# Kernel tuning notes

Hardware: AMD Instinct MI355X
Metric: run time of the kernel (lower is better)

The kernel has to match this reference:

```python
import jax, jax.numpy as jnp
from jax import lax
import numpy as np

STRIDES = (2, 2)
PADDING = 'SAME'
EPS = 1e-05


def setup_inputs() -> dict:
    key = jax.random.key(0)
    k1, k2, k3 = jax.random.split(key, 3)
    x = jax.random.normal(k1, (16, 64, 64, 256), dtype=jnp.float32)
    # flax default conv kernel init ~ lecun_normal; plain normal scaled is fine for a math reference
    kernel = jax.random.normal(k2, (4, 4, 256, 128), dtype=jnp.float32) * 0.05
    bias = jax.random.normal(k3, (128,), dtype=jnp.float32) * 0.01
    alpha = jnp.ones((1,), dtype=jnp.float32)
    return {'x': x, 'kernel': kernel, 'bias': bias, 'alpha': alpha}


def reference(x, kernel, bias, alpha):
    # x: [B, H, W, Cin] NHWC; kernel: [kh, kw, Cin, Cout]
    out_features = kernel.shape[-1]

    # main transposed conv: dot-product map  [B, H*2, W*2, Cout]
    dot = lax.conv_transpose(x, kernel, STRIDES, PADDING, transpose_kernel=False)

    # patch squared-sum map: conv_transpose of x**2 with an all-ones kernel
    # of shape kernel_size + (Cin, 1); broadcast over Cout (same math as jnp.repeat)
    ones_k = jnp.ones(kernel.shape[:-1] + (1,), dtype=kernel.dtype)
    patch_sq = lax.conv_transpose(x * x, ones_k, STRIDES, PADDING, transpose_kernel=False)  # [B, H', W', 1]

    # per-filter kernel squared norm, reduced over (kh, kw, Cin) -> [Cout]
    k_sq = jnp.sum(kernel * kernel, axis=(0, 1, 2))

    # ||x_patch - W||^2 = sum(x^2) + sum(W^2) - 2 * <x, W>
    dist_sq = patch_sq + k_sq - 2.0 * dot

    y = (dot * dot) / (dist_sq + EPS)
    y = y + bias  # broadcast over [B, H', W', Cout]

    nf = jnp.float32(out_features)
    scale = (jnp.sqrt(nf) / jnp.log1p(nf)) ** alpha  # alpha shape (1,) broadcasts
    return y * scale
```

## Files before the change

kernel.cpp:

```cpp
#include <hip/hip_runtime.h>
#include <cstdint>
#include <cstddef>

#define CIN   256
#define COUT  128

typedef float  f32x4  __attribute__((ext_vector_type(4)));
typedef __bf16 bf16x8 __attribute__((ext_vector_type(8)));

#define XPAD_BYTES (16ull*66*66*256*2)
#define WF_OFF     XPAD_BYTES
#define WF_BYTES   (16ull*8*4*128*8*2)
#define SPAD_OFF   (WF_OFF + WF_BYTES)
#define SPAD_BYTES (16ull*66*66*4)
#define KSQ_OFF    (SPAD_OFF + SPAD_BYTES)
#define WS_NEEDED  (KSQ_OFF + 512)

__device__ __forceinline__ unsigned short f2bf(float f) {
  unsigned int u = __float_as_uint(f);
  u += 0x7fffu + ((u >> 16) & 1u);
  return (unsigned short)(u >> 16);
}

__device__ __forceinline__ void async16(const void* lds, const void* g) {
  __builtin_amdgcn_global_load_lds(
      (const __attribute__((address_space(1))) unsigned int*)g,
      (__attribute__((address_space(3))) unsigned int*)lds, 16, 0, 0);
}

__global__ __launch_bounds__(256) void prep_x(
    const float* __restrict__ x, unsigned short* __restrict__ xpad,
    float* __restrict__ spad)
{
  int wave = threadIdx.x >> 6, lane = threadIdx.x & 63;
  int p = blockIdx.x * 4 + wave;
  int b = p / 4356;
  int rem = p - b * 4356;
  int iyp = rem / 66, ixp = rem - iyp * 66;
  bool interior = (iyp >= 1 && iyp <= 64 && ixp >= 1 && ixp <= 64);
  f32x4 v = {0.f, 0.f, 0.f, 0.f};
  if (interior) {
    const float* src = x + (((size_t)b*64 + (iyp-1))*64 + (ixp-1))*CIN + lane*4;
    v = *(const f32x4*)src;
  }
  ushort4 h;
  h.x = f2bf(v.x); h.y = f2bf(v.y); h.z = f2bf(v.z); h.w = f2bf(v.w);
  *(ushort4*)(xpad + (size_t)p*CIN + lane*4) = h;
  float s = v.x*v.x + v.y*v.y + v.z*v.z + v.w*v.w;
  #pragma unroll
  for (int off = 32; off > 0; off >>= 1) s += __shfl_down(s, off);
  if (lane == 0) spad[p] = s;
}

__global__ __launch_bounds__(256) void prep_w2(
    const float* __restrict__ w, unsigned short* __restrict__ wf,
    float* __restrict__ ksq)
{
  int blk = blockIdx.x;
  int tap = blk >> 3, c8 = blk & 7;
  int t = threadIdx.x;
  #pragma unroll
  for (int rr = 0; rr < 2; ++rr) {
    int row = rr*256 + t;
    int q = row >> 7, co = row & 127;
    float s = 0.f;
    union { unsigned short u[8]; uint4 v; } hh;
    #pragma unroll
    for (int e = 0; e < 8; ++e) {
      int ci = c8*32 + q*8 + e;
      float v = w[((size_t)tap*256 + ci)*COUT + co];
      s += v*v;
      hh.u[e] = f2bf(v);
    }
    *(uint4*)(wf + ((size_t)blk*4 + q)*128*8 + (size_t)co*8) = hh.v;
    atomicAdd(ksq + co, s);
  }
}

__global__ __launch_bounds__(256, 2) void yat_main(
    const unsigned short* __restrict__ xpad,
    const unsigned short* __restrict__ wf,
    const float* __restrict__ spad,
    const float* __restrict__ ksq,
    const float* __restrict__ bias,
    const float* __restrict__ alpha,
    float* __restrict__ out)
{
  __shared__ __align__(16) unsigned short xs[2][4224];
  __shared__ float srow[132];

  int orig = blockIdx.x;
  int bid = (orig & 7) * 256 + (orig >> 3);
  int py = bid & 1, u = (bid >> 1) & 63, b = bid >> 7;
  int t = threadIdx.x, wave = t >> 6, lane = t & 63;
  int px = wave >> 1, coh = wave & 1;
  int l15 = lane & 15, l4 = lane >> 4;

  if (t < 132) {
    int r = t / 66, c = t - r*66;
    srow[t] = spad[((size_t)b*66 + (u + py) + r)*66 + c];
  }

  const size_t xrow = ((size_t)b*66 + (u + py)) * 66 * CIN;

  size_t soff0, soff1, tailoff = 0;
  {
    int s = t;
    int a = s / 264; int r2 = s - a*264;
    int q = r2 / 66; int c = r2 - q*66;
    soff0 = xrow + (size_t)(a*66 + c)*CIN + q*8;
    s = 256 + t;
    a = s / 264; r2 = s - a*264;
    q = r2 / 66; c = r2 - q*66;
    soff1 = xrow + (size_t)(a*66 + c)*CIN + q*8;
  }
  if (t < 16) {
    int s2 = 248 + t;
    int q = s2 / 66, c = s2 - q*66;
    tailoff = xrow + (size_t)(66 + c)*CIN + q*8;
  }

  const unsigned short* abase = &xs[0][((size_t)l4*66 + l15 + px)*8];
  const unsigned short* wb =
      wf + ((size_t)l4*128 + coh*64 + l15)*8 + (size_t)(py*4 + px)*32768;

  f32x4 acc[4][4];
  #pragma unroll
  for (int i = 0; i < 4; ++i)
    #pragma unroll
    for (int j = 0; j < 4; ++j)
      acc[i][j] = (f32x4){0.f, 0.f, 0.f, 0.f};

  bf16x8 B0[2][4], B1[2][4];

#define LOAD_B(BANK, AA, C8)                                               \
  {                                                                        \
    _Pragma("unroll")                                                      \
    for (int bb = 0; bb < 2; ++bb)                                         \
      _Pragma("unroll")                                                    \
      for (int nt = 0; nt < 4; ++nt)                                       \
        BANK[bb][nt] = *(const bf16x8*)(                                   \
            wb + (size_t)(AA)*262144 + (size_t)bb*65536 +                  \
                 (size_t)(C8)*4096 + nt*128);                              \
  }

#define STAGE_DMA(NB, CI0)                                                 \
  {                                                                        \
    async16(&xs[NB][(size_t)(0*256 + wave*64)*8], xpad + soff0 + (CI0));   \
    async16(&xs[NB][(size_t)(1*256 + wave*64)*8], xpad + soff1 + (CI0));   \
  }

#define COMPUTE_HALF(BUF, AA, BANK)                                        \
  {                                                                        \
    bf16x8 Af[2][4];                                                       \
    _Pragma("unroll")                                                      \
    for (int bb = 0; bb < 2; ++bb)                                         \
      _Pragma("unroll")                                                    \
      for (int mt = 0; mt < 4; ++mt)                                       \
        Af[bb][mt] = *(const bf16x8*)(abase + (size_t)(BUF)*4224 +         \
            (size_t)((AA)*264 + mt*16 + bb)*8);                            \
    __builtin_amdgcn_s_setprio(1);                                         \
    _Pragma("unroll")                                                      \
    for (int bb = 0; bb < 2; ++bb)                                         \
      _Pragma("unroll")                                                    \
      for (int mt = 0; mt < 4; ++mt)                                       \
        _Pragma("unroll")                                                  \
        for (int nt = 0; nt < 4; ++nt)                                     \
          acc[mt][nt] = __builtin_amdgcn_mfma_f32_16x16x32_bf16(           \
              Af[bb][mt], BANK[bb][nt], acc[mt][nt], 0, 0, 0);             \
    __builtin_amdgcn_s_setprio(0);                                         \
  }

  STAGE_DMA(0, 0);
  uint4 tv;
  if (t < 16) tv = *(const uint4*)(xpad + tailoff);
  LOAD_B(B0, 0, 0);
  if (t < 16) *(uint4*)&xs[0][(size_t)(512 + t)*8] = tv;
  asm volatile("s_waitcnt vmcnt(8) lgkmcnt(0)" ::: "memory");
  __builtin_amdgcn_s_barrier();

  #pragma unroll
  for (int c8 = 0; c8 < 8; ++c8) {
    const int buf = c8 & 1;
    LOAD_B(B1, 1, c8);
    if (c8 < 7) {
      STAGE_DMA(buf ^ 1, (c8 + 1) * 32);
      if (t < 16) tv = *(const uint4*)(xpad + tailoff + (c8 + 1) * 32);
    }
    __builtin_amdgcn_sched_barrier(0);
    COMPUTE_HALF(buf, 0, B0);
    if (c8 < 7) LOAD_B(B0, 0, c8 + 1);
    __builtin_amdgcn_sched_barrier(0);
    COMPUTE_HALF(buf, 1, B1);
    if (c8 < 7) {
      if (t < 16) *(uint4*)&xs[buf ^ 1][(size_t)(512 + t)*8] = tv;
      asm volatile("s_waitcnt vmcnt(8) lgkmcnt(0)" ::: "memory");
      __builtin_amdgcn_s_barrier();
    }
  }

#undef LOAD_B
#undef STAGE_DMA
#undef COMPUTE_HALF

  float scale = powf(sqrtf(128.f) / log1pf(128.f), alpha[0]);
  int oy = 2*u + py;
  float kq[4], bi[4];
  #pragma unroll
  for (int nt = 0; nt < 4; ++nt) {
    int n = coh*64 + nt*16 + l15;
    kq[nt] = ksq[n]; bi[nt] = bias[n];
  }
  size_t orow = ((size_t)b*128 + oy) * 128 * COUT;
  #pragma unroll
  for (int mt = 0; mt < 4; ++mt) {
    #pragma unroll
    for (int r = 0; r < 4; ++r) {
      int v = mt*16 + l4*4 + r;
      float ps = srow[v+px] + srow[v+px+1] + srow[66 + v+px] + srow[66 + v+px+1];
      #pragma unroll
      for (int nt = 0; nt < 4; ++nt) {
        float dot = acc[mt][nt][r];
        float dist = ps + kq[nt] - 2.f*dot + 1e-5f;
        float y = (dot*dot/dist + bi[nt]) * scale;
        int n = coh*64 + nt*16 + l15;
        out[orow + (size_t)(2*v + px)*COUT + n] = y;
      }
    }
  }
}

__global__ __launch_bounds__(256) void fb_ksq(const float* __restrict__ w,
                                              float* __restrict__ ksq) {
  __shared__ float red[256];
  int co = blockIdx.x, t = threadIdx.x;
  float s = 0.f;
  for (int j = t; j < 4096; j += 256) { float v = w[(size_t)j*COUT + co]; s += v*v; }
  red[t] = s; __syncthreads();
  for (int off = 128; off > 0; off >>= 1) {
    if (t < off) red[t] += red[t + off];
    __syncthreads();
  }
  if (t == 0) ksq[co] = red[0];
}

__global__ __launch_bounds__(256) void fb_main(
    const float* __restrict__ x, const float* __restrict__ w,
    const float* __restrict__ bias, const float* __restrict__ alpha,
    const float* __restrict__ ksq, float* __restrict__ out)
{
  size_t idx = (size_t)blockIdx.x * 256 + threadIdx.x;
  int co = (int)(idx & 127);
  int ox = (int)((idx >> 7) & 127);
  int oy = (int)((idx >> 14) & 127);
  int b  = (int)(idx >> 21);
  int py = oy & 1, px = ox & 1, u = oy >> 1, v = ox >> 1;
  float dot = 0.f, ps = 0.f;
  for (int a = 0; a < 2; ++a) {
    int iy = u + py + a - 1;
    if (iy < 0 || iy > 63) continue;
    for (int b2 = 0; b2 < 2; ++b2) {
      int ix = v + px + b2 - 1;
      if (ix < 0 || ix > 63) continue;
      const float* xp = x + (((size_t)b*64 + iy)*64 + ix)*CIN;
      const float* wp = w + ((size_t)((py + 2*a)*4 + (px + 2*b2))*CIN)*COUT + co;
      for (int ci = 0; ci < CIN; ++ci) {
        float xv = xp[ci];
        dot += xv * wp[(size_t)ci*COUT];
        ps  += xv * xv;
      }
    }
  }
  float dist = ps + ksq[co] - 2.f*dot + 1e-5f;
  float scale = powf(sqrtf(128.f) / log1pf(128.f), alpha[0]);
  out[idx] = (dot*dot/dist + bias[co]) * scale;
}

extern "C" void kernel_launch(void* const* d_in, const int* in_sizes, int n_in,
                              void* d_out, int out_size, void* d_ws, size_t ws_size,
                              hipStream_t stream)
{
  const float* x     = (const float*)d_in[0];
  const float* w     = (const float*)d_in[1];
  const float* bias  = (const float*)d_in[2];
  const float* alpha = (const float*)d_in[3];
  float* out = (float*)d_out;

  if (ws_size < WS_NEEDED) {
    float* ksq = (float*)d_ws;
    fb_ksq<<<128, 256, 0, stream>>>(w, ksq);
    fb_main<<<131072, 256, 0, stream>>>(x, w, bias, alpha, ksq, out);
    return;
  }

  unsigned short* xpad = (unsigned short*)d_ws;
  unsigned short* wfp  = (unsigned short*)((char*)d_ws + WF_OFF);
  float* spad = (float*)((char*)d_ws + SPAD_OFF);
  float* ksq  = (float*)((char*)d_ws + KSQ_OFF);

  hipMemsetAsync(ksq, 0, 512, stream);
  prep_x<<<17424, 256, 0, stream>>>(x, xpad, spad);
  prep_w2<<<128, 256, 0, stream>>>(w, wfp, ksq);
  yat_main<<<2048, 256, 0, stream>>>(xpad, wfp, spad, ksq, bias, alpha, out);
}
```

Before: 121.3 us.

## Pre-swizzle padded input into MFMA fragment layout and drop LDS staging

The x-preprocessing kernel now writes one padded row per block through LDS into a [b][row][ci/8][col][8] bf16 layout. The main GEMM kernel can then load A fragments directly from global memory with 16-byte vector loads, which removes the LDS double buffer, the async DMA and the per-stage barriers. Occupancy hint rises to 3 blocks per CU. In exchange, A operands are served from global memory and cache instead of shared LDS, so overlapping rows read by neighbouring blocks rely on L2 hits and latency is only hidden by occupancy.

```diff
diff --git a/kernel.cpp b/kernel.cpp
--- a/kernel.cpp
+++ b/kernel.cpp
@@ -8,8 +8,8 @@
 typedef float  f32x4  __attribute__((ext_vector_type(4)));
 typedef __bf16 bf16x8 __attribute__((ext_vector_type(8)));
 
-#define XPAD_BYTES (16ull*66*66*256*2)
-#define WF_OFF     XPAD_BYTES
+#define XF_BYTES   (16ull*66*32*66*8*2)
+#define WF_OFF     XF_BYTES
 #define WF_BYTES   (16ull*8*4*128*8*2)
 #define SPAD_OFF   (WF_OFF + WF_BYTES)
 #define SPAD_BYTES (16ull*66*66*4)
@@ -22,34 +22,50 @@
   return (unsigned short)(u >> 16);
 }
 
-__device__ __forceinline__ void async16(const void* lds, const void* g) {
-  __builtin_amdgcn_global_load_lds(
-      (const __attribute__((address_space(1))) unsigned int*)g,
-      (__attribute__((address_space(3))) unsigned int*)lds, 16, 0, 0);
-}
-
-__global__ __launch_bounds__(256) void prep_x(
-    const float* __restrict__ x, unsigned short* __restrict__ xpad,
+__global__ __launch_bounds__(256) void prep_x2(
+    const float* __restrict__ x, unsigned short* __restrict__ xf,
     float* __restrict__ spad)
 {
-  int wave = threadIdx.x >> 6, lane = threadIdx.x & 63;
-  int p = blockIdx.x * 4 + wave;
-  int b = p / 4356;
-  int rem = p - b * 4356;
-  int iyp = rem / 66, ixp = rem - iyp * 66;
-  bool interior = (iyp >= 1 && iyp <= 64 && ixp >= 1 && ixp <= 64);
-  f32x4 v = {0.f, 0.f, 0.f, 0.f};
+  __shared__ __align__(16) unsigned short lw[66*258 + 8];
+  int blk = blockIdx.x;
+  int b = blk / 66, row = blk - b*66;
+  int t = threadIdx.x, wave = t >> 6, lane = t & 63;
+  bool interior = (row >= 1 && row <= 64);
+  int iy = row - 1;
+
   if (interior) {
-    const float* src = x + (((size_t)b*64 + (iyp-1))*64 + (ixp-1))*CIN + lane*4;
-    v = *(const f32x4*)src;
-  }
-  ushort4 h;
-  h.x = f2bf(v.x); h.y = f2bf(v.y); h.z = f2bf(v.z); h.w = f2bf(v.w);
-  *(ushort4*)(xpad + (size_t)p*CIN + lane*4) = h;
-  float s = v.x*v.x + v.y*v.y + v.z*v.z + v.w*v.w;
-  #pragma unroll
-  for (int off = 32; off > 0; off >>= 1) s += __shfl_down(s, off);
-  if (lane == 0) spad[p] = s;
+    #pragma unroll
+    for (int p = 0; p < 16; ++p) {
+      int cx = 4*p + wave;
+      f32x4 v = *(const f32x4*)(x + (((size_t)b*64 + iy)*64 + cx)*CIN + lane*4);
+      ushort4 h; h.x=f2bf(v.x); h.y=f2bf(v.y); h.z=f2bf(v.z); h.w=f2bf(v.w);
+      *(ushort4*)&lw[(size_t)(cx+1)*258 + lane*4] = h;
+      float s = v.x*v.x + v.y*v.y + v.z*v.z + v.w*v.w;
+      #pragma unroll
+      for (int off = 32; off > 0; off >>= 1) s += __shfl_down(s, off);
+      if (lane == 0) spad[(size_t)blk*66 + cx + 1] = s;
+    }
+    if (t < 2) spad[(size_t)blk*66 + t*65] = 0.f;
+    if (t < 64) {
+      int col = (t & 1) * 65, q = t >> 1;
+      *(uint4*)&lw[(size_t)col*258 + q*8] = (uint4){0,0,0,0};
+    }
+  } else {
+    if (t < 66) spad[(size_t)blk*66 + t] = 0.f;
+  }
+  __syncthreads();
+
+  size_t obase = (size_t)blk * 32 * 66 * 8;
+  #pragma unroll
+  for (int k = 0; k < 9; ++k) {
+    int un = k*256 + t;
+    if (un < 2112) {
+      int q = un / 66, col = un - q*66;
+      uint4 val = interior ? *(uint4*)&lw[(size_t)col*258 + q*8]
+                           : (uint4){0u,0u,0u,0u};
+      *(uint4*)(xf + obase + (size_t)un*8) = val;
+    }
+  }
 }
 
 __global__ __launch_bounds__(256) void prep_w2(
@@ -77,8 +93,8 @@
   }
 }
 
-__global__ __launch_bounds__(256, 2) void yat_main(
-    const unsigned short* __restrict__ xpad,
+__global__ __launch_bounds__(256, 3) void yat_main(
+    const unsigned short* __restrict__ xf,
     const unsigned short* __restrict__ wf,
     const float* __restrict__ spad,
     const float* __restrict__ ksq,
@@ -86,7 +102,6 @@
     const float* __restrict__ alpha,
     float* __restrict__ out)
 {
-  __shared__ __align__(16) unsigned short xs[2][4224];
   __shared__ float srow[132];
 
   int orig = blockIdx.x;
@@ -101,26 +116,8 @@
     srow[t] = spad[((size_t)b*66 + (u + py) + r)*66 + c];
   }
 
-  const size_t xrow = ((size_t)b*66 + (u + py)) * 66 * CIN;
-
-  size_t soff0, soff1, tailoff = 0;
-  {
-    int s = t;
-    int a = s / 264; int r2 = s - a*264;
-    int q = r2 / 66; int c = r2 - q*66;
-    soff0 = xrow + (size_t)(a*66 + c)*CIN + q*8;
-    s = 256 + t;
-    a = s / 264; r2 = s - a*264;
-    q = r2 / 66; c = r2 - q*66;
-    soff1 = xrow + (size_t)(a*66 + c)*CIN + q*8;
-  }
-  if (t < 16) {
-    int s2 = 248 + t;
-    int q = s2 / 66, c = s2 - q*66;
-    tailoff = xrow + (size_t)(66 + c)*CIN + q*8;
-  }
-
-  const unsigned short* abase = &xs[0][((size_t)l4*66 + l15 + px)*8];
+  const unsigned short* ab =
+      xf + ((((size_t)b*66 + (u + py))*32 + l4)*66 + px + l15)*8;
   const unsigned short* wb =
       wf + ((size_t)l4*128 + coh*64 + l15)*8 + (size_t)(py*4 + px)*32768;
 
@@ -144,64 +141,42 @@
                  (size_t)(C8)*4096 + nt*128);                              \
   }
 
-#define STAGE_DMA(NB, CI0)                                                 \
+#define COMPUTE_HALF(AA, BANK, C8)                                         \
   {                                                                        \
-    async16(&xs[NB][(size_t)(0*256 + wave*64)*8], xpad + soff0 + (CI0));   \
-    async16(&xs[NB][(size_t)(1*256 + wave*64)*8], xpad + soff1 + (CI0));   \
-  }
-
-#define COMPUTE_HALF(BUF, AA, BANK)                                        \
-  {                                                                        \
-    bf16x8 Af[2][4];                                                       \
     _Pragma("unroll")                                                      \
-    for (int bb = 0; bb < 2; ++bb)                                         \
+    for (int bb = 0; bb < 2; ++bb) {                                       \
+      bf16x8 Af[4];                                                        \
       _Pragma("unroll")                                                    \
       for (int mt = 0; mt < 4; ++mt)                                       \
-        Af[bb][mt] = *(const bf16x8*)(abase + (size_t)(BUF)*4224 +         \
-            (size_t)((AA)*264 + mt*16 + bb)*8);                            \
-    __builtin_amdgcn_s_setprio(1);                                         \
-    _Pragma("unroll")                                                      \
-    for (int bb = 0; bb < 2; ++bb)                                         \
+        Af[mt] = *(const bf16x8*)(ab + (size_t)(AA)*16896 +                \
+            (size_t)(C8)*2112 + (mt*16 + bb)*8);                           \
+      __builtin_amdgcn_s_setprio(1);                                       \
       _Pragma("unroll")                                                    \
       for (int mt = 0; mt < 4; ++mt)                                       \
         _Pragma("unroll")                                                  \
         for (int nt = 0; nt < 4; ++nt)                                     \
           acc[mt][nt] = __builtin_amdgcn_mfma_f32_16x16x32_bf16(           \
-              Af[bb][mt], BANK[bb][nt], acc[mt][nt], 0, 0, 0);             \
-    __builtin_amdgcn_s_setprio(0);                                         \
-  }
-
-  STAGE_DMA(0, 0);
-  uint4 tv;
-  if (t < 16) tv = *(const uint4*)(xpad + tailoff);
+              Af[mt], BANK[bb][nt], acc[mt][nt], 0, 0, 0);                 \
+      __builtin_amdgcn_s_setprio(0);                                       \
+    }                                                                      \
+  }
+
   LOAD_B(B0, 0, 0);
-  if (t < 16) *(uint4*)&xs[0][(size_t)(512 + t)*8] = tv;
-  asm volatile("s_waitcnt vmcnt(8) lgkmcnt(0)" ::: "memory");
-  __builtin_amdgcn_s_barrier();
-
   #pragma unroll
   for (int c8 = 0; c8 < 8; ++c8) {
-    const int buf = c8 & 1;
     LOAD_B(B1, 1, c8);
-    if (c8 < 7) {
-      STAGE_DMA(buf ^ 1, (c8 + 1) * 32);
-      if (t < 16) tv = *(const uint4*)(xpad + tailoff + (c8 + 1) * 32);
-    }
     __builtin_amdgcn_sched_barrier(0);
-    COMPUTE_HALF(buf, 0, B0);
+    COMPUTE_HALF(0, B0, c8);
     if (c8 < 7) LOAD_B(B0, 0, c8 + 1);
     __builtin_amdgcn_sched_barrier(0);
-    COMPUTE_HALF(buf, 1, B1);
-    if (c8 < 7) {
-      if (t < 16) *(uint4*)&xs[buf ^ 1][(size_t)(512 + t)*8] = tv;
-      asm volatile("s_waitcnt vmcnt(8) lgkmcnt(0)" ::: "memory");
-      __builtin_amdgcn_s_barrier();
-    }
+    COMPUTE_HALF(1, B1, c8);
+    __builtin_amdgcn_sched_barrier(0);
   }
 
 #undef LOAD_B
-#undef STAGE_DMA
 #undef COMPUTE_HALF
+
+  __syncthreads();
 
   float scale = powf(sqrtf(128.f) / log1pf(128.f), alpha[0]);
   int oy = 2*u + py;
@@ -293,13 +268,13 @@
     return;
   }
 
-  unsigned short* xpad = (unsigned short*)d_ws;
-  unsigned short* wfp  = (unsigned short*)((char*)d_ws + WF_OFF);
+  unsigned short* xfp = (unsigned short*)d_ws;
+  unsigned short* wfp = (unsigned short*)((char*)d_ws + WF_OFF);
   float* spad = (float*)((char*)d_ws + SPAD_OFF);
   float* ksq  = (float*)((char*)d_ws + KSQ_OFF);
 
   hipMemsetAsync(ksq, 0, 512, stream);
-  prep_x<<<17424, 256, 0, stream>>>(x, xpad, spad);
+  prep_x2<<<1056, 256, 0, stream>>>(x, xfp, spad);
   prep_w2<<<128, 256, 0, stream>>>(w, wfp, ksq);
-  yat_main<<<2048, 256, 0, stream>>>(xpad, wfp, spad, ksq, bias, alpha, out);
-}
+  yat_main<<<2048, 256, 0, stream>>>(xfp, wfp, spad, ksq, bias, alpha, out);
+}
```

Result: no change. 121.5 us (+0.2%).

## Triple-buffer LDS staging with hand-scheduled inline-asm loads in GEMM main loop

Applied to the files above, without the earlier changes.

The main transposed-conv GEMM loop moves from double to triple LDS buffering. It is fully unrolled with inline-asm global_load_dwordx4 and ds_read_b128 plus explicit vmcnt and lgkmcnt waits, so x-tile DMA runs two stages ahead and the weight fragments are prefetched. The kernel-norm computation moves from atomics in prep_w2, which needed a preceding memset, to the dedicated reduction kernel. The tighter schedule is meant to hide global latency better, at the cost of more LDS per block, which could reduce occupancy, and fragile hand-counted wait values.

```diff
diff --git a/kernel.cpp b/kernel.cpp
--- a/kernel.cpp
+++ b/kernel.cpp
@@ -7,6 +7,7 @@
 
 typedef float  f32x4  __attribute__((ext_vector_type(4)));
 typedef __bf16 bf16x8 __attribute__((ext_vector_type(8)));
+typedef unsigned int u32x4 __attribute__((ext_vector_type(4)));
 
 #define XPAD_BYTES (16ull*66*66*256*2)
 #define WF_OFF     XPAD_BYTES
@@ -53,8 +54,7 @@
 }
 
 __global__ __launch_bounds__(256) void prep_w2(
-    const float* __restrict__ w, unsigned short* __restrict__ wf,
-    float* __restrict__ ksq)
+    const float* __restrict__ w, unsigned short* __restrict__ wf)
 {
   int blk = blockIdx.x;
   int tap = blk >> 3, c8 = blk & 7;
@@ -63,18 +63,28 @@
   for (int rr = 0; rr < 2; ++rr) {
     int row = rr*256 + t;
     int q = row >> 7, co = row & 127;
-    float s = 0.f;
     union { unsigned short u[8]; uint4 v; } hh;
     #pragma unroll
     for (int e = 0; e < 8; ++e) {
       int ci = c8*32 + q*8 + e;
-      float v = w[((size_t)tap*256 + ci)*COUT + co];
-      s += v*v;
-      hh.u[e] = f2bf(v);
+      hh.u[e] = f2bf(w[((size_t)tap*256 + ci)*COUT + co]);
     }
     *(uint4*)(wf + ((size_t)blk*4 + q)*128*8 + (size_t)co*8) = hh.v;
-    atomicAdd(ksq + co, s);
-  }
+  }
+}
+
+__global__ __launch_bounds__(256) void fb_ksq(const float* __restrict__ w,
+                                              float* __restrict__ ksq) {
+  __shared__ float red[256];
+  int co = blockIdx.x, t = threadIdx.x;
+  float s = 0.f;
+  for (int j = t; j < 4096; j += 256) { float v = w[(size_t)j*COUT + co]; s += v*v; }
+  red[t] = s; __syncthreads();
+  for (int off = 128; off > 0; off >>= 1) {
+    if (t < off) red[t] += red[t + off];
+    __syncthreads();
+  }
+  if (t == 0) ksq[co] = red[0];
 }
 
 __global__ __launch_bounds__(256, 2) void yat_main(
@@ -86,7 +96,7 @@
     const float* __restrict__ alpha,
     float* __restrict__ out)
 {
-  __shared__ __align__(16) unsigned short xs[2][4224];
+  __shared__ __align__(16) unsigned short xs[3][4224];
   __shared__ float srow[132];
 
   int orig = blockIdx.x;
@@ -103,7 +113,7 @@
 
   const size_t xrow = ((size_t)b*66 + (u + py)) * 66 * CIN;
 
-  size_t soff0, soff1, tailoff = 0;
+  size_t soff0, soff1, tailoff;
   {
     int s = t;
     int a = s / 264; int r2 = s - a*264;
@@ -113,14 +123,13 @@
     a = s / 264; r2 = s - a*264;
     q = r2 / 66; c = r2 - q*66;
     soff1 = xrow + (size_t)(a*66 + c)*CIN + q*8;
-  }
-  if (t < 16) {
-    int s2 = 248 + t;
-    int q = s2 / 66, c = s2 - q*66;
-    tailoff = xrow + (size_t)(66 + c)*CIN + q*8;
-  }
-
-  const unsigned short* abase = &xs[0][((size_t)l4*66 + l15 + px)*8];
+    int s2 = 248 + (t & 15);
+    int q2 = s2 / 66, c2 = s2 - q2*66;
+    tailoff = xrow + (size_t)(66 + c2)*CIN + q2*8;
+  }
+
+  unsigned ab_lds = (unsigned)(unsigned long long)(&xs[0][0])
+                    + (unsigned)((l4*66 + l15 + px) * 16);
   const unsigned short* wb =
       wf + ((size_t)l4*128 + coh*64 + l15)*8 + (size_t)(py*4 + px)*32768;
 
@@ -131,77 +140,127 @@
     for (int j = 0; j < 4; ++j)
       acc[i][j] = (f32x4){0.f, 0.f, 0.f, 0.f};
 
-  bf16x8 B0[2][4], B1[2][4];
-
-#define LOAD_B(BANK, AA, C8)                                               \
+  u32x4 B0[2][4], B1[2][4];
+  u32x4 Af[2][4];
+  u32x4 tvA, tvB;
+
+#define SB  __builtin_amdgcn_sched_barrier(0)
+#define BAR __builtin_amdgcn_s_barrier()
+#define VMW(N) do { asm volatile("s_waitcnt vmcnt(" #N ")" ::: "memory"); SB; } while (0)
+#define LGK(N) do { asm volatile("s_waitcnt lgkmcnt(" #N ")" ::: "memory"); SB; } while (0)
+
+#define GLB(dst, base, off)                                                \
+  asm volatile("global_load_dwordx4 %0, %1, off offset:%c2"                \
+               : "=v"(dst) : "v"(base), "i"(off))
+
+#define DSR(dst, off)                                                      \
+  asm volatile("ds_read_b128 %0, %1 offset:%c2"                            \
+               : "=v"(dst) : "v"(ab_lds), "i"(off))
+
+#define STAGE(BUF, K, TV)                                                  \
+  {                                                                        \
+    async16(&xs[BUF][(size_t)(0*256 + wave*64)*8], xpad + soff0 + (K)*32); \
+    async16(&xs[BUF][(size_t)(1*256 + wave*64)*8], xpad + soff1 + (K)*32); \
+    SB;                                                                    \
+    GLB(TV, (const char*)(xpad + tailoff + (K)*32), 0);                    \
+    SB;                                                                    \
+  }
+
+#define TAILW(BUF, TV)                                                     \
+  { if (t < 16) *((u32x4*)&xs[BUF][(size_t)(512 + t)*8]) = TV; }
+
+#define ISSUEB(BANK, AA, C8)                                               \
+  {                                                                        \
+    const char* pb0 = (const char*)wb + (AA)*524288 + (C8)*8192;           \
+    const char* pb1 = pb0 + 131072;                                        \
+    GLB(BANK[0][0], pb0, 0);   GLB(BANK[0][1], pb0, 256);                  \
+    GLB(BANK[0][2], pb0, 512); GLB(BANK[0][3], pb0, 768);                  \
+    GLB(BANK[1][0], pb1, 0);   GLB(BANK[1][1], pb1, 256);                  \
+    GLB(BANK[1][2], pb1, 512); GLB(BANK[1][3], pb1, 768);                  \
+    SB;                                                                    \
+  }
+
+#define MFMA16(BB, BANK)                                                   \
   {                                                                        \
     _Pragma("unroll")                                                      \
-    for (int bb = 0; bb < 2; ++bb)                                         \
+    for (int mt = 0; mt < 4; ++mt)                                         \
       _Pragma("unroll")                                                    \
       for (int nt = 0; nt < 4; ++nt)                                       \
-        BANK[bb][nt] = *(const bf16x8*)(                                   \
-            wb + (size_t)(AA)*262144 + (size_t)bb*65536 +                  \
-                 (size_t)(C8)*4096 + nt*128);                              \
-  }
-
-#define STAGE_DMA(NB, CI0)                                                 \
+        acc[mt][nt] = __builtin_amdgcn_mfma_f32_16x16x32_bf16(             \
+            __builtin_bit_cast(bf16x8, Af[BB][mt]),                        \
+            __builtin_bit_cast(bf16x8, BANK[BB][nt]),                      \
+            acc[mt][nt], 0, 0, 0);                                         \
+  }
+
+#define HALF(N, BUF, A, BANK)                                              \
   {                                                                        \
-    async16(&xs[NB][(size_t)(0*256 + wave*64)*8], xpad + soff0 + (CI0));   \
-    async16(&xs[NB][(size_t)(1*256 + wave*64)*8], xpad + soff1 + (CI0));   \
-  }
-
-#define COMPUTE_HALF(BUF, AA, BANK)                                        \
-  {                                                                        \
-    bf16x8 Af[2][4];                                                       \
-    _Pragma("unroll")                                                      \
-    for (int bb = 0; bb < 2; ++bb)                                         \
-      _Pragma("unroll")                                                    \
-      for (int mt = 0; mt < 4; ++mt)                                       \
-        Af[bb][mt] = *(const bf16x8*)(abase + (size_t)(BUF)*4224 +         \
-            (size_t)((AA)*264 + mt*16 + bb)*8);                            \
+    VMW(N);                                                                \
+    DSR(Af[0][0], (BUF)*8448 + (A)*4224 + 0);                              \
+    DSR(Af[0][1], (BUF)*8448 + (A)*4224 + 256);                            \
+    DSR(Af[0][2], (BUF)*8448 + (A)*4224 + 512);                            \
+    DSR(Af[0][3], (BUF)*8448 + (A)*4224 + 768);                            \
+    DSR(Af[1][0], (BUF)*8448 + (A)*4224 + 16);                             \
+    DSR(Af[1][1], (BUF)*8448 + (A)*4224 + 272);                            \
+    DSR(Af[1][2], (BUF)*8448 + (A)*4224 + 528);                            \
+    DSR(Af[1][3], (BUF)*8448 + (A)*4224 + 784);                            \
+    LGK(4);                                                                \
     __builtin_amdgcn_s_setprio(1);                                         \
-    _Pragma("unroll")                                                      \
-    for (int bb = 0; bb < 2; ++bb)                                         \
-      _Pragma("unroll")                                                    \
-      for (int mt = 0; mt < 4; ++mt)                                       \
-        _Pragma("unroll")                                                  \
-        for (int nt = 0; nt < 4; ++nt)                                     \
-          acc[mt][nt] = __builtin_amdgcn_mfma_f32_16x16x32_bf16(           \
-              Af[bb][mt], BANK[bb][nt], acc[mt][nt], 0, 0, 0);             \
+    MFMA16(0, BANK);                                                       \
+    LGK(0);                                                                \
+    MFMA16(1, BANK);                                                       \
     __builtin_amdgcn_s_setprio(0);                                         \
-  }
-
-  STAGE_DMA(0, 0);
-  uint4 tv;
-  if (t < 16) tv = *(const uint4*)(xpad + tailoff);
-  LOAD_B(B0, 0, 0);
-  if (t < 16) *(uint4*)&xs[0][(size_t)(512 + t)*8] = tv;
-  asm volatile("s_waitcnt vmcnt(8) lgkmcnt(0)" ::: "memory");
-  __builtin_amdgcn_s_barrier();
-
-  #pragma unroll
-  for (int c8 = 0; c8 < 8; ++c8) {
-    const int buf = c8 & 1;
-    LOAD_B(B1, 1, c8);
-    if (c8 < 7) {
-      STAGE_DMA(buf ^ 1, (c8 + 1) * 32);
-      if (t < 16) tv = *(const uint4*)(xpad + tailoff + (c8 + 1) * 32);
-    }
-    __builtin_amdgcn_sched_barrier(0);
-    COMPUTE_HALF(buf, 0, B0);
-    if (c8 < 7) LOAD_B(B0, 0, c8 + 1);
-    __builtin_amdgcn_sched_barrier(0);
-    COMPUTE_HALF(buf, 1, B1);
-    if (c8 < 7) {
-      if (t < 16) *(uint4*)&xs[buf ^ 1][(size_t)(512 + t)*8] = tv;
-      asm volatile("s_waitcnt vmcnt(8) lgkmcnt(0)" ::: "memory");
-      __builtin_amdgcn_s_barrier();
-    }
-  }
-
-#undef LOAD_B
-#undef STAGE_DMA
-#undef COMPUTE_HALF
+    SB;                                                                    \
+  }
+
+  SB;
+  STAGE(0, 0, tvA);
+  STAGE(1, 1, tvB);
+  ISSUEB(B0, 0, 0);
+  ISSUEB(B1, 1, 0);
+  VMW(19);
+  TAILW(0, tvA); LGK(0); BAR; SB;
+
+  STAGE(2, 2, tvA);
+  HALF(11, 0, 0, B0);  ISSUEB(B0, 0, 1);
+  HALF(11, 0, 1, B1);  ISSUEB(B1, 1, 1);
+  TAILW(1, tvB); LGK(0); BAR; SB;
+  STAGE(0, 3, tvB);
+  HALF(11, 1, 0, B0);  ISSUEB(B0, 0, 2);
+  HALF(11, 1, 1, B1);  ISSUEB(B1, 1, 2);
+  TAILW(2, tvA); LGK(0); BAR; SB;
+  STAGE(1, 4, tvA);
+  HALF(11, 2, 0, B0);  ISSUEB(B0, 0, 3);
+  HALF(11, 2, 1, B1);  ISSUEB(B1, 1, 3);
+  TAILW(0, tvB); LGK(0); BAR; SB;
+  STAGE(2, 5, tvB);
+  HALF(11, 0, 0, B0);  ISSUEB(B0, 0, 4);
+  HALF(11, 0, 1, B1);  ISSUEB(B1, 1, 4);
+  TAILW(1, tvA); LGK(0); BAR; SB;
+  STAGE(0, 6, tvA);
+  HALF(11, 1, 0, B0);  ISSUEB(B0, 0, 5);
+  HALF(11, 1, 1, B1);  ISSUEB(B1, 1, 5);
+  TAILW(2, tvB); LGK(0); BAR; SB;
+  STAGE(1, 7, tvB);
+  HALF(11, 2, 0, B0);  ISSUEB(B0, 0, 6);
+  HALF(11, 2, 1, B1);  ISSUEB(B1, 1, 6);
+  TAILW(0, tvA); LGK(0); BAR; SB;
+  HALF(8, 0, 0, B0);   ISSUEB(B0, 0, 7);
+  HALF(8, 0, 1, B1);   ISSUEB(B1, 1, 7);
+  TAILW(1, tvB); LGK(0); BAR; SB;
+  HALF(8, 1, 0, B0);
+  HALF(0, 1, 1, B1);
+
+#undef SB
+#undef BAR
+#undef VMW
+#undef LGK
+#undef GLB
+#undef DSR
+#undef STAGE
+#undef TAILW
+#undef ISSUEB
+#undef MFMA16
+#undef HALF
 
   float scale = powf(sqrtf(128.f) / log1pf(128.f), alpha[0]);
   int oy = 2*u + py;
@@ -228,20 +287,6 @@
       }
     }
   }
-}
-
-__global__ __launch_bounds__(256) void fb_ksq(const float* __restrict__ w,
-                                              float* __restrict__ ksq) {
-  __shared__ float red[256];
-  int co = blockIdx.x, t = threadIdx.x;
-  float s = 0.f;
-  for (int j = t; j < 4096; j += 256) { float v = w[(size_t)j*COUT + co]; s += v*v; }
-  red[t] = s; __syncthreads();
-  for (int off = 128; off > 0; off >>= 1) {
-    if (t < off) red[t] += red[t + off];
-    __syncthreads();
-  }
-  if (t == 0) ksq[co] = red[0];
 }
 
 __global__ __launch_bounds__(256) void fb_main(
@@ -298,8 +343,8 @@
   float* spad = (float*)((char*)d_ws + SPAD_OFF);
   float* ksq  = (float*)((char*)d_ws + KSQ_OFF);
 
-  hipMemsetAsync(ksq, 0, 512, stream);
+  fb_ksq<<<128, 256, 0, stream>>>(w, ksq);
   prep_x<<<17424, 256, 0, stream>>>(x, xpad, spad);
-  prep_w2<<<128, 256, 0, stream>>>(w, wfp, ksq);
+  prep_w2<<<128, 256, 0, stream>>>(w, wfp);
   yat_main<<<2048, 256, 0, stream>>>(xpad, wfp, spad, ksq, bias, alpha, out);
 }
```

Result: faster. 113.8 us (-6.2%).
